# Kernel tuning notes

Measured on AMD Instinct MI355X. Metric: run time of the kernel, lower is better.

## Reference

```python
import jax, jax.numpy as jnp
import numpy as np

D_MODEL = 1024
NUM_HEADS = 16
HEAD_DIM = D_MODEL // NUM_HEADS
SCALE = HEAD_DIM ** -0.5


def setup_inputs() -> dict:
    key = jax.random.key(0)
    ks = jax.random.split(key, 5)
    B, N = 2, 2048
    x = jax.random.normal(ks[0], (B, N, D_MODEL), dtype=jnp.float32)
    # Linear params, torch layout: weight [out, in], bias [out]
    w_qkv = jax.random.normal(ks[1], (3 * D_MODEL, D_MODEL), dtype=jnp.float32) * (D_MODEL ** -0.5)
    b_qkv = jax.random.normal(ks[2], (3 * D_MODEL,), dtype=jnp.float32) * 0.02
    w_proj = jax.random.normal(ks[3], (D_MODEL, D_MODEL), dtype=jnp.float32) * (D_MODEL ** -0.5)
    b_proj = jax.random.normal(ks[4], (D_MODEL,), dtype=jnp.float32) * 0.02
    return {"x": x, "w_qkv": w_qkv, "b_qkv": b_qkv, "w_proj": w_proj, "b_proj": b_proj}


def reference(x, w_qkv, b_qkv, w_proj, b_proj):
    B, N, C = x.shape
    qkv = x @ w_qkv.T + b_qkv                      # [B, N, 3C]
    qkv = qkv.reshape(B, N, 3, NUM_HEADS, HEAD_DIM)
    qkv = jnp.transpose(qkv, (2, 0, 3, 1, 4))      # [3, B, H, N, d]
    q, k, v = qkv[0], qkv[1], qkv[2]
    attn = jnp.einsum('bhnd,bhmd->bhnm', q, k) * SCALE  # [B, H, N, N]
    attn = jax.nn.softmax(attn, axis=-1)
    # dropout is identity in eval mode
    out = jnp.einsum('bhnm,bhmd->bhnd', attn, v)   # [B, H, N, d]
    out = jnp.transpose(out, (0, 2, 1, 3)).reshape(B, N, C)
    return out @ w_proj.T + b_proj
```

## Files before the change

kernel.cpp:

```cpp
#include <hip/hip_runtime.h>

typedef short short8 __attribute__((ext_vector_type(8)));
typedef short short4v __attribute__((ext_vector_type(4)));
typedef float f32x4 __attribute__((ext_vector_type(4)));
typedef float float4v __attribute__((ext_vector_type(4)));
typedef int int4v __attribute__((ext_vector_type(4)));
typedef int int2v __attribute__((ext_vector_type(2)));

__device__ __forceinline__ short f2bf(float f) {
  union { float f; unsigned u; } v; v.f = f;
  unsigned r = v.u + 0x7FFFu + ((v.u >> 16) & 1u);
  return (short)(r >> 16);
}

__device__ __forceinline__ unsigned cvtpk_bf16(float lo, float hi) {
  unsigned r;
  asm("v_cvt_pk_bf16_f32 %0, %1, %2" : "=v"(r) : "v"(lo), "v"(hi));
  return r;
}

#define GLD16(gp, lp)                                                   \
  __builtin_amdgcn_global_load_lds(                                     \
      (const __attribute__((address_space(1))) void*)(gp),              \
      (__attribute__((address_space(3))) void*)(lp), 16, 0, 0)

#define QSCALE 0.18033688011112042f

__global__ __launch_bounds__(256) void cvt_all(
    const float* __restrict__ x, const float* __restrict__ wq, const float* __restrict__ wp,
    short* __restrict__ xb, short* __restrict__ wqb, short* __restrict__ wpb) {
  int i = blockIdx.x * 256 + threadIdx.x;
  const float* s; short* d; int off;
  if (i < 1048576)      { s = x;  d = xb;  off = i; }
  else if (i < 1835008) { s = wq; d = wqb; off = i - 1048576; }
  else                  { s = wp; d = wpb; off = i - 1835008; }
  float4v v = ((const float4v*)s)[off];
  short4v o;
  o.x = f2bf(v.x); o.y = f2bf(v.y); o.z = f2bf(v.z); o.w = f2bf(v.w);
  ((short4v*)d)[off] = o;
}

template <int MODE>
__global__ __launch_bounds__(256, 3) void gemm_bt(
    const short* __restrict__ A, const short* __restrict__ Bw,
    const float* __restrict__ bias,
    short* __restrict__ qo, short* __restrict__ ko, short* __restrict__ vto,
    float* __restrict__ outf) {
  __shared__ short As[3][128 * 32];
  __shared__ short Bs[3][128 * 32];
  const int t = threadIdx.x;
  const int lane = t & 63, wid = t >> 6;
  const int g = lane >> 4, l15 = lane & 15;
  const int wr = (wid >> 1) * 64, wc = (wid & 1) * 64;
  const int bid = blockIdx.x;
  const int bm0 = ((bid & 7) * 4 + ((bid >> 3) & 3)) * 128;
  const int bn0 = (bid >> 5) * 128;

  const int sr = t >> 2;
  const int csrc = (t & 3) ^ ((t >> 3) & 3);

  const int gx = (g ^ ((l15 >> 1) & 3)) << 4;
  int aoff[4], boff[4];
#pragma unroll
  for (int f = 0; f < 4; ++f) {
    aoff[f] = (wr + f * 16 + l15) * 64 + gx;
    boff[f] = (wc + f * 16 + l15) * 64 + gx;
  }

  f32x4 acc[4][4] = {};

  auto stage = [&](int offB, int k0) {
#pragma unroll
    for (int i = 0; i < 2; ++i) {
      int row = i * 64 + sr;
      char* ldsA = (char*)&As[0][0] + offB + (i * 256 + (t & ~63)) * 16;
      char* ldsB = (char*)&Bs[0][0] + offB + (i * 256 + (t & ~63)) * 16;
      GLD16(A + (size_t)(bm0 + row) * 1024 + k0 + csrc * 8, ldsA);
      GLD16(Bw + (size_t)(bn0 + row) * 1024 + k0 + csrc * 8, ldsB);
    }
  };

  stage(0, 0);
  stage(8192, 32);
  stage(16384, 64);
  int off = 0;

  for (int it = 0; it < 32; ++it) {
    if (it < 30)       asm volatile("s_waitcnt vmcnt(8)" ::: "memory");
    else if (it == 30) asm volatile("s_waitcnt vmcnt(4)" ::: "memory");
    else               asm volatile("s_waitcnt vmcnt(0)" ::: "memory");
    __builtin_amdgcn_s_barrier();
    __builtin_amdgcn_sched_barrier(0);
    const char* AsB = (const char*)&As[0][0] + off;
    const char* BsB = (const char*)&Bs[0][0] + off;
    short8 a[4], b[4];
#pragma unroll
    for (int mi = 0; mi < 4; ++mi) a[mi] = *(const short8*)(AsB + aoff[mi]);
#pragma unroll
    for (int ni = 0; ni < 4; ++ni) b[ni] = *(const short8*)(BsB + boff[ni]);
#pragma unroll
    for (int mi = 0; mi < 4; ++mi)
#pragma unroll
      for (int ni = 0; ni < 4; ++ni)
        acc[mi][ni] = __builtin_amdgcn_mfma_f32_16x16x32_bf16(a[mi], b[ni], acc[mi][ni], 0, 0, 0);
    __builtin_amdgcn_sched_barrier(0);
    __builtin_amdgcn_s_barrier();
    __builtin_amdgcn_sched_barrier(0);
    if (it + 3 < 32) stage(off, (it + 3) * 32);
    off = (off == 16384) ? 0 : off + 8192;
  }

  if constexpr (MODE == 0) {
    const int which = bn0 >> 10;
    if (which == 2) {
#pragma unroll
      for (int mi = 0; mi < 4; ++mi) {
#pragma unroll
        for (int ni = 0; ni < 4; ++ni) {
          int gcol = bn0 + wc + ni * 16 + l15;
          int w1 = gcol & 1023;
          int h = w1 >> 6, dd = w1 & 63;
          float bv = bias[gcol];
          int grow0 = bm0 + wr + mi * 16 + g * 4;
          int b_ = grow0 >> 11, n0 = grow0 & 2047;
          int bh = b_ * 16 + h;
          int nl = n0 & 63;
          int np = (n0 & ~63) | (nl & 32) | ((nl & 12) << 1) | ((nl & 16) >> 2);
          int2v pk;
          pk.x = (int)cvtpk_bf16(acc[mi][ni][0] + bv, acc[mi][ni][1] + bv);
          pk.y = (int)cvtpk_bf16(acc[mi][ni][2] + bv, acc[mi][ni][3] + bv);
          *(int2v*)(vto + ((size_t)bh * 64 + dd) * 2048 + np) = pk;
        }
      }
    } else {
      short* dst = (which == 0) ? qo : ko;
      const float sc = (which == 0) ? QSCALE : 1.0f;
#pragma unroll
      for (int mi = 0; mi < 4; ++mi) {
#pragma unroll
        for (int ni = 0; ni < 4; ++ni) {
          int gcol = bn0 + wc + ni * 16 + l15;
          int w1 = gcol & 1023;
          int h = w1 >> 6, dd = w1 & 63;
          float bv = bias[gcol];
#pragma unroll
          for (int r = 0; r < 4; ++r) {
            int grow = bm0 + wr + mi * 16 + g * 4 + r;
            int b_ = grow >> 11, n = grow & 2047;
            int bh = b_ * 16 + h;
            dst[((size_t)bh * 2048 + n) * 64 + dd] = f2bf((acc[mi][ni][r] + bv) * sc);
          }
        }
      }
    }
  } else {
#pragma unroll
    for (int mi = 0; mi < 4; ++mi) {
#pragma unroll
      for (int ni = 0; ni < 4; ++ni) {
        int gcol = bn0 + wc + ni * 16 + l15;
        float bv = bias[gcol];
#pragma unroll
        for (int r = 0; r < 4; ++r) {
          int grow = bm0 + wr + mi * 16 + g * 4 + r;
          outf[(size_t)grow * 1024 + gcol] = acc[mi][ni][r] + bv;
        }
      }
    }
  }
}

__global__ __launch_bounds__(256, 2) void attn_fused(
    const short* __restrict__ Qg, const short* __restrict__ Kg,
    const short* __restrict__ Vtg, short* __restrict__ AO) {
  __shared__ short Ks[4][64 * 64];
  __shared__ short Vs[4][64 * 64];
  const int bid = blockIdx.x;
  const int bh = bid & 31, qt = bid >> 5;
  const int t = threadIdx.x, wid = t >> 6, lane = t & 63;
  const int g = lane >> 4, l15 = lane & 15;
  const int q0w = qt * 128 + wid * 32;
  const short* qb = Qg + ((size_t)bh * 2048 + q0w) * 64;
  const short* kb = Kg + (size_t)bh * 2048 * 64;
  const short* vb = Vtg + (size_t)bh * 64 * 2048;

  const int srow = t >> 3;
  const int ssub = (t & 7) ^ (srow & 7);
  const short* ksrc0 = kb + srow * 64 + ssub * 8;
  const short* vsrc0 = vb + (size_t)srow * 2048 + ssub * 8;

  const int swz = (l15 & 7) << 4;
  int foff[2][4];
#pragma unroll
  for (int kk = 0; kk < 2; ++kk)
#pragma unroll
    for (int f = 0; f < 4; ++f)
      foff[kk][f] = ((f * 16 + l15) * 128 + kk * 64 + g * 16) ^ swz;

  short8 bq[2][2];
#pragma unroll
  for (int qf = 0; qf < 2; ++qf)
#pragma unroll
    for (int kk = 0; kk < 2; ++kk)
      bq[qf][kk] = *(const short8*)(qb + (qf * 16 + l15) * 64 + kk * 32 + g * 8);

  auto stageP = [&](int buf, int p) {
    const int n0 = p * 128;
#pragma unroll
    for (int sub = 0; sub < 2; ++sub) {
      const int nn = n0 + sub * 64;
      char* ldsK = (char*)&Ks[buf * 2 + sub][0] + wid * 1024;
      char* ldsV = (char*)&Vs[buf * 2 + sub][0] + wid * 1024;
#pragma unroll
      for (int i = 0; i < 2; ++i) {
        GLD16(ksrc0 + (size_t)(nn + i * 32) * 64, ldsK + i * 4096);
        GLD16(vsrc0 + (size_t)i * 32 * 2048 + nn, ldsV + i * 4096);
      }
    }
  };

  stageP(0, 0);
  stageP(1, 1);

  f32x4 acc[2][4] = {};
  float mrun[2] = {-3.0e38f, -3.0e38f}, lrun[2] = {0.f, 0.f};

  for (int p = 0; p < 16; ++p) {
    if (p == 15) asm volatile("s_waitcnt vmcnt(0)" ::: "memory");
    else         asm volatile("s_waitcnt vmcnt(8)" ::: "memory");
    __builtin_amdgcn_s_barrier();
    __builtin_amdgcn_sched_barrier(0);
    const int buf = p & 1;

#pragma unroll
    for (int sub = 0; sub < 2; ++sub) {
      const char* KsB = (const char*)&Ks[buf * 2 + sub][0];
      const char* VsB = (const char*)&Vs[buf * 2 + sub][0];

      f32x4 s[2][4] = {};
#pragma unroll
      for (int kk = 0; kk < 2; ++kk) {
        short8 ak[4];
#pragma unroll
        for (int kf = 0; kf < 4; ++kf) ak[kf] = *(const short8*)(KsB + foff[kk][kf]);
#pragma unroll
        for (int kf = 0; kf < 4; ++kf)
#pragma unroll
          for (int qf = 0; qf < 2; ++qf)
            s[qf][kf] = __builtin_amdgcn_mfma_f32_16x16x32_bf16(ak[kf], bq[qf][kk], s[qf][kf], 0, 0, 0);
      }

      float pm[2];
#pragma unroll
      for (int qf = 0; qf < 2; ++qf) {
        float m0 = fmaxf(s[qf][0][0], s[qf][0][1]);
        m0 = fmaxf(fmaxf(m0, s[qf][0][2]), s[qf][0][3]);
#pragma unroll
        for (int kf = 1; kf < 4; ++kf) {
          m0 = fmaxf(fmaxf(m0, s[qf][kf][0]), s[qf][kf][1]);
          m0 = fmaxf(fmaxf(m0, s[qf][kf][2]), s[qf][kf][3]);
        }
        float x = fmaxf(m0, __shfl_xor(m0, 16));
        pm[qf] = fmaxf(x, __shfl_xor(x, 32));
      }

      if (!__all((pm[0] - mrun[0] <= 8.f) && (pm[1] - mrun[1] <= 8.f))) {
#pragma unroll
        for (int qf = 0; qf < 2; ++qf) {
          float mn = fmaxf(mrun[qf], pm[qf]);
          float alpha = __builtin_amdgcn_exp2f(mrun[qf] - mn);
          mrun[qf] = mn;
          lrun[qf] *= alpha;
#pragma unroll
          for (int df = 0; df < 4; ++df)
#pragma unroll
            for (int r = 0; r < 4; ++r) acc[qf][df][r] *= alpha;
        }
      }

      unsigned wpk[2][4][2];
#pragma unroll
      for (int qf = 0; qf < 2; ++qf) {
        float rs = 0.f;
        float pp[4][4];
#pragma unroll
        for (int kf = 0; kf < 4; ++kf)
#pragma unroll
          for (int r = 0; r < 4; ++r) {
            pp[kf][r] = __builtin_amdgcn_exp2f(s[qf][kf][r] - mrun[qf]);
            rs += pp[kf][r];
          }
        rs += __shfl_xor(rs, 16);
        rs += __shfl_xor(rs, 32);
        lrun[qf] += rs;
#pragma unroll
        for (int kf = 0; kf < 4; ++kf)
#pragma unroll
          for (int h = 0; h < 2; ++h)
            wpk[qf][kf][h] = cvtpk_bf16(pp[kf][2 * h], pp[kf][2 * h + 1]);
      }

#pragma unroll
      for (int kk = 0; kk < 2; ++kk) {
        short8 av[4];
#pragma unroll
        for (int df = 0; df < 4; ++df) av[df] = *(const short8*)(VsB + foff[kk][df]);
#pragma unroll
        for (int qf = 0; qf < 2; ++qf) {
          union { int4v i; short8 s; } pv;
          pv.i[0] = (int)wpk[qf][2 * kk][0];
          pv.i[1] = (int)wpk[qf][2 * kk][1];
          pv.i[2] = (int)wpk[qf][2 * kk + 1][0];
          pv.i[3] = (int)wpk[qf][2 * kk + 1][1];
#pragma unroll
          for (int df = 0; df < 4; ++df)
            acc[qf][df] = __builtin_amdgcn_mfma_f32_16x16x32_bf16(av[df], pv.s, acc[qf][df], 0, 0, 0);
        }
      }
    }

    __builtin_amdgcn_sched_barrier(0);
    __builtin_amdgcn_s_barrier();
    __builtin_amdgcn_sched_barrier(0);
    if (p + 2 < 16) stageP(buf, p + 2);
  }

  const int b_ = bh >> 4, h = bh & 15;
#pragma unroll
  for (int qf = 0; qf < 2; ++qf) {
    const float inv = 1.0f / lrun[qf];
    short* outp = AO + ((size_t)b_ * 2048 + q0w + qf * 16 + l15) * 1024 + h * 64 + g * 4;
#pragma unroll
    for (int df = 0; df < 4; ++df) {
      short4v o;
#pragma unroll
      for (int r = 0; r < 4; ++r) o[r] = f2bf(acc[qf][df][r] * inv);
      *(short4v*)(outp + df * 16) = o;
    }
  }
}

extern "C" void kernel_launch(void* const* d_in, const int* in_sizes, int n_in,
                              void* d_out, int out_size, void* d_ws, size_t ws_size,
                              hipStream_t stream) {
  const float* x = (const float*)d_in[0];
  const float* w_qkv = (const float*)d_in[1];
  const float* b_qkv = (const float*)d_in[2];
  const float* w_proj = (const float*)d_in[3];
  const float* b_proj = (const float*)d_in[4];
  float* out = (float*)d_out;
  char* ws = (char*)d_ws;

  short* xb    = (short*)(ws + (size_t)0);
  short* wqkvb = (short*)(ws + ((size_t)8 << 20));
  short* wprojb= (short*)(ws + ((size_t)14 << 20));
  short* qb    = (short*)(ws + ((size_t)16 << 20));
  short* kb    = (short*)(ws + ((size_t)24 << 20));
  short* vtb   = (short*)(ws + ((size_t)32 << 20));
  short* aob   = (short*)(ws + ((size_t)40 << 20));

  cvt_all<<<8192, 256, 0, stream>>>(x, w_qkv, w_proj, xb, wqkvb, wprojb);
  gemm_bt<0><<<768, 256, 0, stream>>>(xb, wqkvb, b_qkv, qb, kb, vtb, nullptr);
  attn_fused<<<512, 256, 0, stream>>>(qb, kb, vtb, aob);
  gemm_bt<1><<<256, 256, 0, stream>>>(aob, wprojb, b_proj, nullptr, nullptr, nullptr, out);
}
```

Baseline: 115.7 us.

## Split attention KV sequence across wave pairs and merge partial softmax in LDS

Doubles the attention block to 512 threads, with each pair of waves sharing the same 32 queries but handling opposite halves of the key/value sequence (split-K flash attention). K loads are issued by waves 0-3 and V loads by waves 4-7. At the end, partial accumulators and running max/sum are exchanged through LDS and merged with rescaling. The aim is more waves in flight to hide latency and shorter per-wave serial loops. The cost is an extra LDS merge step, and the larger block with 64KB of shared memory may limit how many blocks fit per CU.

```diff
diff --git a/kernel.cpp b/kernel.cpp
--- a/kernel.cpp
+++ b/kernel.cpp
@@ -170,24 +170,26 @@
   }
 }
 
-__global__ __launch_bounds__(256, 2) void attn_fused(
+__global__ __launch_bounds__(512, 4) void attn_fused(
     const short* __restrict__ Qg, const short* __restrict__ Kg,
     const short* __restrict__ Vtg, short* __restrict__ AO) {
-  __shared__ short Ks[4][64 * 64];
-  __shared__ short Vs[4][64 * 64];
+  __shared__ char smem[65536];
+#define KSB(hf, buf) (smem + ((hf) * 2 + (buf)) * 8192)
+#define VSB(hf, buf) (smem + 32768 + ((hf) * 2 + (buf)) * 8192)
   const int bid = blockIdx.x;
   const int bh = bid & 31, qt = bid >> 5;
   const int t = threadIdx.x, wid = t >> 6, lane = t & 63;
   const int g = lane >> 4, l15 = lane & 15;
-  const int q0w = qt * 128 + wid * 32;
+  const int qg = wid >> 1, hf = wid & 1;
+  const int q0w = qt * 128 + qg * 32;
   const short* qb = Qg + ((size_t)bh * 2048 + q0w) * 64;
   const short* kb = Kg + (size_t)bh * 2048 * 64;
   const short* vb = Vtg + (size_t)bh * 64 * 2048;
 
-  const int srow = t >> 3;
-  const int ssub = (t & 7) ^ (srow & 7);
-  const short* ksrc0 = kb + srow * 64 + ssub * 8;
-  const short* vsrc0 = vb + (size_t)srow * 2048 + ssub * 8;
+  const int sr = (t & 255) >> 3;
+  const int ssub = (t & 7) ^ ((t >> 3) & 7);
+  const short* ksrc0 = kb + sr * 64 + ssub * 8;
+  const short* vsrc0 = vb + (size_t)sr * 2048 + ssub * 8;
 
   const int swz = (l15 & 7) << 4;
   int foff[2][4];
@@ -205,17 +207,20 @@
       bq[qf][kk] = *(const short8*)(qb + (qf * 16 + l15) * 64 + kk * 32 + g * 8);
 
   auto stageP = [&](int buf, int p) {
-    const int n0 = p * 128;
-#pragma unroll
-    for (int sub = 0; sub < 2; ++sub) {
-      const int nn = n0 + sub * 64;
-      char* ldsK = (char*)&Ks[buf * 2 + sub][0] + wid * 1024;
-      char* ldsV = (char*)&Vs[buf * 2 + sub][0] + wid * 1024;
-#pragma unroll
-      for (int i = 0; i < 2; ++i) {
-        GLD16(ksrc0 + (size_t)(nn + i * 32) * 64, ldsK + i * 4096);
-        GLD16(vsrc0 + (size_t)i * 32 * 2048 + nn, ldsV + i * 4096);
-      }
+    if (wid < 4) {
+#pragma unroll
+      for (int h2 = 0; h2 < 2; ++h2)
+#pragma unroll
+        for (int i = 0; i < 2; ++i)
+          GLD16(ksrc0 + (size_t)(h2 * 1024 + p * 64 + i * 32) * 64,
+                KSB(h2, buf) + i * 4096 + wid * 1024);
+    } else {
+#pragma unroll
+      for (int h2 = 0; h2 < 2; ++h2)
+#pragma unroll
+        for (int i = 0; i < 2; ++i)
+          GLD16(vsrc0 + (size_t)(i * 32) * 2048 + h2 * 1024 + p * 64,
+                VSB(h2, buf) + i * 4096 + (wid - 4) * 1024);
     }
   };
 
@@ -227,117 +232,138 @@
 
   for (int p = 0; p < 16; ++p) {
     if (p == 15) asm volatile("s_waitcnt vmcnt(0)" ::: "memory");
-    else         asm volatile("s_waitcnt vmcnt(8)" ::: "memory");
+    else         asm volatile("s_waitcnt vmcnt(4)" ::: "memory");
     __builtin_amdgcn_s_barrier();
     __builtin_amdgcn_sched_barrier(0);
-    const int buf = p & 1;
-
-#pragma unroll
-    for (int sub = 0; sub < 2; ++sub) {
-      const char* KsB = (const char*)&Ks[buf * 2 + sub][0];
-      const char* VsB = (const char*)&Vs[buf * 2 + sub][0];
-
-      f32x4 s[2][4] = {};
-#pragma unroll
-      for (int kk = 0; kk < 2; ++kk) {
-        short8 ak[4];
-#pragma unroll
-        for (int kf = 0; kf < 4; ++kf) ak[kf] = *(const short8*)(KsB + foff[kk][kf]);
-#pragma unroll
-        for (int kf = 0; kf < 4; ++kf)
-#pragma unroll
-          for (int qf = 0; qf < 2; ++qf)
-            s[qf][kf] = __builtin_amdgcn_mfma_f32_16x16x32_bf16(ak[kf], bq[qf][kk], s[qf][kf], 0, 0, 0);
-      }
-
-      float pm[2];
+    const char* KsB = (const char*)KSB(hf, p & 1);
+    const char* VsB = (const char*)VSB(hf, p & 1);
+
+    f32x4 s[2][4] = {};
+#pragma unroll
+    for (int kk = 0; kk < 2; ++kk) {
+      short8 ak[4];
+#pragma unroll
+      for (int kf = 0; kf < 4; ++kf) ak[kf] = *(const short8*)(KsB + foff[kk][kf]);
+#pragma unroll
+      for (int kf = 0; kf < 4; ++kf)
+#pragma unroll
+        for (int qf = 0; qf < 2; ++qf)
+          s[qf][kf] = __builtin_amdgcn_mfma_f32_16x16x32_bf16(ak[kf], bq[qf][kk], s[qf][kf], 0, 0, 0);
+    }
+
+    float pm[2];
+#pragma unroll
+    for (int qf = 0; qf < 2; ++qf) {
+      float m0 = fmaxf(s[qf][0][0], s[qf][0][1]);
+      m0 = fmaxf(fmaxf(m0, s[qf][0][2]), s[qf][0][3]);
+#pragma unroll
+      for (int kf = 1; kf < 4; ++kf) {
+        m0 = fmaxf(fmaxf(m0, s[qf][kf][0]), s[qf][kf][1]);
+        m0 = fmaxf(fmaxf(m0, s[qf][kf][2]), s[qf][kf][3]);
+      }
+      float x = fmaxf(m0, __shfl_xor(m0, 16));
+      pm[qf] = fmaxf(x, __shfl_xor(x, 32));
+    }
+
+    if (!__all((pm[0] - mrun[0] <= 8.f) && (pm[1] - mrun[1] <= 8.f))) {
 #pragma unroll
       for (int qf = 0; qf < 2; ++qf) {
-        float m0 = fmaxf(s[qf][0][0], s[qf][0][1]);
-        m0 = fmaxf(fmaxf(m0, s[qf][0][2]), s[qf][0][3]);
-#pragma unroll
-        for (int kf = 1; kf < 4; ++kf) {
-          m0 = fmaxf(fmaxf(m0, s[qf][kf][0]), s[qf][kf][1]);
-          m0 = fmaxf(fmaxf(m0, s[qf][kf][2]), s[qf][kf][3]);
+        float mn = fmaxf(mrun[qf], pm[qf]);
+        float alpha = __builtin_amdgcn_exp2f(mrun[qf] - mn);
+        mrun[qf] = mn;
+        lrun[qf] *= alpha;
+#pragma unroll
+        for (int df = 0; df < 4; ++df)
+#pragma unroll
+          for (int r = 0; r < 4; ++r) acc[qf][df][r] *= alpha;
+      }
+    }
+
+    unsigned wpk[2][4][2];
+#pragma unroll
+    for (int qf = 0; qf < 2; ++qf) {
+      float rs = 0.f;
+      float pp[4][4];
+#pragma unroll
+      for (int kf = 0; kf < 4; ++kf)
+#pragma unroll
+        for (int r = 0; r < 4; ++r) {
+          pp[kf][r] = __builtin_amdgcn_exp2f(s[qf][kf][r] - mrun[qf]);
+          rs += pp[kf][r];
         }
-        float x = fmaxf(m0, __shfl_xor(m0, 16));
-        pm[qf] = fmaxf(x, __shfl_xor(x, 32));
-      }
-
-      if (!__all((pm[0] - mrun[0] <= 8.f) && (pm[1] - mrun[1] <= 8.f))) {
-#pragma unroll
-        for (int qf = 0; qf < 2; ++qf) {
-          float mn = fmaxf(mrun[qf], pm[qf]);
-          float alpha = __builtin_amdgcn_exp2f(mrun[qf] - mn);
-          mrun[qf] = mn;
-          lrun[qf] *= alpha;
-#pragma unroll
-          for (int df = 0; df < 4; ++df)
-#pragma unroll
-            for (int r = 0; r < 4; ++r) acc[qf][df][r] *= alpha;
-        }
-      }
-
-      unsigned wpk[2][4][2];
+      rs += __shfl_xor(rs, 16);
+      rs += __shfl_xor(rs, 32);
+      lrun[qf] += rs;
+#pragma unroll
+      for (int kf = 0; kf < 4; ++kf)
+#pragma unroll
+        for (int h2 = 0; h2 < 2; ++h2)
+          wpk[qf][kf][h2] = cvtpk_bf16(pp[kf][2 * h2], pp[kf][2 * h2 + 1]);
+    }
+
+#pragma unroll
+    for (int kk = 0; kk < 2; ++kk) {
+      short8 av[4];
+#pragma unroll
+      for (int df = 0; df < 4; ++df) av[df] = *(const short8*)(VsB + foff[kk][df]);
 #pragma unroll
       for (int qf = 0; qf < 2; ++qf) {
-        float rs = 0.f;
-        float pp[4][4];
-#pragma unroll
-        for (int kf = 0; kf < 4; ++kf)
-#pragma unroll
-          for (int r = 0; r < 4; ++r) {
-            pp[kf][r] = __builtin_amdgcn_exp2f(s[qf][kf][r] - mrun[qf]);
-            rs += pp[kf][r];
-          }
-        rs += __shfl_xor(rs, 16);
-        rs += __shfl_xor(rs, 32);
-        lrun[qf] += rs;
-#pragma unroll
-        for (int kf = 0; kf < 4; ++kf)
-#pragma unroll
-          for (int h = 0; h < 2; ++h)
-            wpk[qf][kf][h] = cvtpk_bf16(pp[kf][2 * h], pp[kf][2 * h + 1]);
-      }
-
-#pragma unroll
-      for (int kk = 0; kk < 2; ++kk) {
-        short8 av[4];
-#pragma unroll
-        for (int df = 0; df < 4; ++df) av[df] = *(const short8*)(VsB + foff[kk][df]);
-#pragma unroll
-        for (int qf = 0; qf < 2; ++qf) {
-          union { int4v i; short8 s; } pv;
-          pv.i[0] = (int)wpk[qf][2 * kk][0];
-          pv.i[1] = (int)wpk[qf][2 * kk][1];
-          pv.i[2] = (int)wpk[qf][2 * kk + 1][0];
-          pv.i[3] = (int)wpk[qf][2 * kk + 1][1];
-#pragma unroll
-          for (int df = 0; df < 4; ++df)
-            acc[qf][df] = __builtin_amdgcn_mfma_f32_16x16x32_bf16(av[df], pv.s, acc[qf][df], 0, 0, 0);
-        }
+        union { int4v i; short8 s; } pv;
+        pv.i[0] = (int)wpk[qf][2 * kk][0];
+        pv.i[1] = (int)wpk[qf][2 * kk][1];
+        pv.i[2] = (int)wpk[qf][2 * kk + 1][0];
+        pv.i[3] = (int)wpk[qf][2 * kk + 1][1];
+#pragma unroll
+        for (int df = 0; df < 4; ++df)
+          acc[qf][df] = __builtin_amdgcn_mfma_f32_16x16x32_bf16(av[df], pv.s, acc[qf][df], 0, 0, 0);
       }
     }
 
     __builtin_amdgcn_sched_barrier(0);
     __builtin_amdgcn_s_barrier();
     __builtin_amdgcn_sched_barrier(0);
-    if (p + 2 < 16) stageP(buf, p + 2);
-  }
-
-  const int b_ = bh >> 4, h = bh & 15;
-#pragma unroll
-  for (int qf = 0; qf < 2; ++qf) {
-    const float inv = 1.0f / lrun[qf];
-    short* outp = AO + ((size_t)b_ * 2048 + q0w + qf * 16 + l15) * 1024 + h * 64 + g * 4;
-#pragma unroll
-    for (int df = 0; df < 4; ++df) {
-      short4v o;
-#pragma unroll
-      for (int r = 0; r < 4; ++r) o[r] = f2bf(acc[qf][df][r] * inv);
-      *(short4v*)(outp + df * 16) = o;
-    }
-  }
+    if (p + 2 < 16) stageP(p & 1, p + 2);
+  }
+
+  float* cacc = (float*)smem;
+  float* cml = (float*)(smem + 4 * 64 * 33 * 4);
+  __syncthreads();
+  if (hf == 1) {
+    float* pa = cacc + (qg * 64 + lane) * 33;
+#pragma unroll
+    for (int qf = 0; qf < 2; ++qf)
+#pragma unroll
+      for (int df = 0; df < 4; ++df)
+#pragma unroll
+        for (int r = 0; r < 4; ++r) pa[qf * 16 + df * 4 + r] = acc[qf][df][r];
+    float* pl = cml + (qg * 64 + lane) * 4;
+    pl[0] = mrun[0]; pl[1] = lrun[0]; pl[2] = mrun[1]; pl[3] = lrun[1];
+  }
+  __syncthreads();
+  if (hf == 0) {
+    const float* pa = cacc + (qg * 64 + lane) * 33;
+    const float* pl = cml + (qg * 64 + lane) * 4;
+    const int b_ = bh >> 4, h = bh & 15;
+#pragma unroll
+    for (int qf = 0; qf < 2; ++qf) {
+      float m1 = pl[qf * 2], l1 = pl[qf * 2 + 1];
+      float M = fmaxf(mrun[qf], m1);
+      float a0 = __builtin_amdgcn_exp2f(mrun[qf] - M);
+      float a1 = __builtin_amdgcn_exp2f(m1 - M);
+      float inv = 1.0f / (lrun[qf] * a0 + l1 * a1);
+      short* outp = AO + ((size_t)b_ * 2048 + q0w + qf * 16 + l15) * 1024 + h * 64 + g * 4;
+#pragma unroll
+      for (int df = 0; df < 4; ++df) {
+        short4v o;
+#pragma unroll
+        for (int r = 0; r < 4; ++r)
+          o[r] = f2bf((acc[qf][df][r] * a0 + pa[qf * 16 + df * 4 + r] * a1) * inv);
+        *(short4v*)(outp + df * 16) = o;
+      }
+    }
+  }
+#undef KSB
+#undef VSB
 }
 
 extern "C" void kernel_launch(void* const* d_in, const int* in_sizes, int n_in,
@@ -361,6 +387,6 @@
 
   cvt_all<<<8192, 256, 0, stream>>>(x, w_qkv, w_proj, xb, wqkvb, wprojb);
   gemm_bt<0><<<768, 256, 0, stream>>>(xb, wqkvb, b_qkv, qb, kb, vtb, nullptr);
-  attn_fused<<<512, 256, 0, stream>>>(qb, kb, vtb, aob);
+  attn_fused<<<512, 512, 0, stream>>>(qb, kb, vtb, aob);
   gemm_bt<1><<<256, 256, 0, stream>>>(aob, wprojb, b_proj, nullptr, nullptr, nullptr, out);
 }
```

New measurement: 135.6 us. 17.3% more time.

## Use 256x256-tile 512-thread GEMM for QKV projection with double-buffered LDS

Applied to the files above, without the earlier changes.

Replaces the 128x128-tile QKV GEMM with a new kernel using 256x256 tiles, 8 waves, K-step 64 and a 128KB double-buffered LDS pipeline. Staging of the next k-tile is interleaved with the MFMA sub-loops, with explicit vmcnt waits and setprio around the MFMAs. The larger tile raises arithmetic intensity and cuts global traffic per FLOP. The grid drops to 192 blocks, below the 256 CUs, so the GPU is under-occupied and fewer blocks hide latency. The output projection is split out into its own non-templated kernel.

```diff
diff --git a/kernel.cpp b/kernel.cpp
--- a/kernel.cpp
+++ b/kernel.cpp
@@ -40,12 +40,134 @@
   ((short4v*)d)[off] = o;
 }
 
-template <int MODE>
-__global__ __launch_bounds__(256, 3) void gemm_bt(
+__global__ __launch_bounds__(512, 2) void gemm256(
     const short* __restrict__ A, const short* __restrict__ Bw,
     const float* __restrict__ bias,
-    short* __restrict__ qo, short* __restrict__ ko, short* __restrict__ vto,
-    float* __restrict__ outf) {
+    short* __restrict__ qo, short* __restrict__ ko, short* __restrict__ vto) {
+  __shared__ char lds[131072];
+  const int t = threadIdx.x;
+  const int lane = t & 63, wid = t >> 6;
+  const int g = lane >> 4, l15 = lane & 15;
+  const int wr = wid >> 2, wc = wid & 3;
+  const int bid = blockIdx.x;
+  const int bm0 = ((bid & 7) * 2 + ((bid >> 3) & 1)) * 256;
+  const int bn0 = (bid >> 4) * 256;
+
+  const int srow = t >> 3;
+  const int ssub = (t & 7) ^ ((t >> 3) & 7);
+
+  const int swz = (l15 & 7) << 4;
+  int inrow[2];
+  inrow[0] = (g * 16) ^ swz;
+  inrow[1] = (64 + g * 16) ^ swz;
+  const int bRow0 = (wc & 1) * 64;
+
+  f32x4 acc[8][4] = {};
+
+  auto stageHT = [&](int b, int kt, int ht) {
+    const int isB = ht >> 1, hh = ht & 1;
+    const short* mat = isB ? Bw : A;
+    const int base = isB ? bn0 : bm0;
+    const short* src = mat + (size_t)(base + hh * 128 + srow) * 1024 + kt * 64 + ssub * 8;
+    char* dst = lds + b * 65536 + isB * 32768 + hh * 16384 + t * 16;
+    GLD16(src, dst);
+    GLD16(src + 64 * 1024, dst + 8192);
+  };
+
+#pragma unroll
+  for (int ht = 0; ht < 4; ++ht) stageHT(0, 0, ht);
+
+  for (int k = 0; k < 16; ++k) {
+    const int buf = k & 1;
+    const char* Ab = lds + buf * 65536 + wr * 16384;
+    const char* Bb = lds + buf * 65536 + 32768 + (wc >> 1) * 16384;
+    short8 bB[4][2];
+#pragma unroll
+    for (int mp = 0; mp < 4; ++mp) {
+      if (k + 1 < 16) stageHT(buf ^ 1, k + 1, mp);
+      __builtin_amdgcn_sched_barrier(0);
+      if (mp == 0) {
+        if (k + 1 < 16) asm volatile("s_waitcnt vmcnt(2)" ::: "memory");
+        else            asm volatile("s_waitcnt vmcnt(0)" ::: "memory");
+        __builtin_amdgcn_s_barrier();
+        __builtin_amdgcn_sched_barrier(0);
+#pragma unroll
+        for (int n = 0; n < 4; ++n)
+#pragma unroll
+          for (int kk = 0; kk < 2; ++kk)
+            bB[n][kk] = *(const short8*)(Bb + (bRow0 + n * 16 + l15) * 128 + inrow[kk]);
+      }
+      short8 aA[2][2];
+#pragma unroll
+      for (int mm = 0; mm < 2; ++mm)
+#pragma unroll
+        for (int kk = 0; kk < 2; ++kk)
+          aA[mm][kk] = *(const short8*)(Ab + ((mp * 2 + mm) * 16 + l15) * 128 + inrow[kk]);
+      __builtin_amdgcn_s_setprio(1);
+#pragma unroll
+      for (int mm = 0; mm < 2; ++mm)
+#pragma unroll
+        for (int n = 0; n < 4; ++n)
+#pragma unroll
+          for (int kk = 0; kk < 2; ++kk)
+            acc[mp * 2 + mm][n] = __builtin_amdgcn_mfma_f32_16x16x32_bf16(
+                aA[mm][kk], bB[n][kk], acc[mp * 2 + mm][n], 0, 0, 0);
+      __builtin_amdgcn_s_setprio(0);
+      if (mp == 3) {
+        __builtin_amdgcn_sched_barrier(0);
+        __builtin_amdgcn_s_barrier();
+        __builtin_amdgcn_sched_barrier(0);
+      }
+    }
+  }
+
+  const int which = bn0 >> 10;
+  if (which == 2) {
+#pragma unroll
+    for (int m = 0; m < 8; ++m) {
+#pragma unroll
+      for (int n = 0; n < 4; ++n) {
+        int gcol = bn0 + wc * 64 + n * 16 + l15;
+        int w1 = gcol & 1023;
+        int h = w1 >> 6, dd = w1 & 63;
+        float bv = bias[gcol];
+        int grow0 = bm0 + wr * 128 + m * 16 + g * 4;
+        int b_ = grow0 >> 11, n0 = grow0 & 2047;
+        int bh = b_ * 16 + h;
+        int nl = n0 & 63;
+        int np = (n0 & ~63) | (nl & 32) | ((nl & 12) << 1) | ((nl & 16) >> 2);
+        int2v pk;
+        pk.x = (int)cvtpk_bf16(acc[m][n][0] + bv, acc[m][n][1] + bv);
+        pk.y = (int)cvtpk_bf16(acc[m][n][2] + bv, acc[m][n][3] + bv);
+        *(int2v*)(vto + ((size_t)bh * 64 + dd) * 2048 + np) = pk;
+      }
+    }
+  } else {
+    short* dst = (which == 0) ? qo : ko;
+    const float sc = (which == 0) ? QSCALE : 1.0f;
+#pragma unroll
+    for (int m = 0; m < 8; ++m) {
+#pragma unroll
+      for (int n = 0; n < 4; ++n) {
+        int gcol = bn0 + wc * 64 + n * 16 + l15;
+        int w1 = gcol & 1023;
+        int h = w1 >> 6, dd = w1 & 63;
+        float bv = bias[gcol];
+#pragma unroll
+        for (int r = 0; r < 4; ++r) {
+          int grow = bm0 + wr * 128 + m * 16 + g * 4 + r;
+          int b_ = grow >> 11, n2 = grow & 2047;
+          int bh = b_ * 16 + h;
+          dst[((size_t)bh * 2048 + n2) * 64 + dd] = f2bf((acc[m][n][r] + bv) * sc);
+        }
+      }
+    }
+  }
+}
+
+__global__ __launch_bounds__(256, 3) void gemm_proj(
+    const short* __restrict__ A, const short* __restrict__ Bw,
+    const float* __restrict__ bias, float* __restrict__ outf) {
   __shared__ short As[3][128 * 32];
   __shared__ short Bs[3][128 * 32];
   const int t = threadIdx.x;
@@ -110,61 +232,16 @@
     off = (off == 16384) ? 0 : off + 8192;
   }
 
-  if constexpr (MODE == 0) {
-    const int which = bn0 >> 10;
-    if (which == 2) {
-#pragma unroll
-      for (int mi = 0; mi < 4; ++mi) {
-#pragma unroll
-        for (int ni = 0; ni < 4; ++ni) {
-          int gcol = bn0 + wc + ni * 16 + l15;
-          int w1 = gcol & 1023;
-          int h = w1 >> 6, dd = w1 & 63;
-          float bv = bias[gcol];
-          int grow0 = bm0 + wr + mi * 16 + g * 4;
-          int b_ = grow0 >> 11, n0 = grow0 & 2047;
-          int bh = b_ * 16 + h;
-          int nl = n0 & 63;
-          int np = (n0 & ~63) | (nl & 32) | ((nl & 12) << 1) | ((nl & 16) >> 2);
-          int2v pk;
-          pk.x = (int)cvtpk_bf16(acc[mi][ni][0] + bv, acc[mi][ni][1] + bv);
-          pk.y = (int)cvtpk_bf16(acc[mi][ni][2] + bv, acc[mi][ni][3] + bv);
-          *(int2v*)(vto + ((size_t)bh * 64 + dd) * 2048 + np) = pk;
-        }
-      }
-    } else {
-      short* dst = (which == 0) ? qo : ko;
-      const float sc = (which == 0) ? QSCALE : 1.0f;
-#pragma unroll
-      for (int mi = 0; mi < 4; ++mi) {
-#pragma unroll
-        for (int ni = 0; ni < 4; ++ni) {
-          int gcol = bn0 + wc + ni * 16 + l15;
-          int w1 = gcol & 1023;
-          int h = w1 >> 6, dd = w1 & 63;
-          float bv = bias[gcol];
-#pragma unroll
-          for (int r = 0; r < 4; ++r) {
-            int grow = bm0 + wr + mi * 16 + g * 4 + r;
-            int b_ = grow >> 11, n = grow & 2047;
-            int bh = b_ * 16 + h;
-            dst[((size_t)bh * 2048 + n) * 64 + dd] = f2bf((acc[mi][ni][r] + bv) * sc);
-          }
-        }
-      }
-    }
-  } else {
-#pragma unroll
-    for (int mi = 0; mi < 4; ++mi) {
-#pragma unroll
-      for (int ni = 0; ni < 4; ++ni) {
-        int gcol = bn0 + wc + ni * 16 + l15;
-        float bv = bias[gcol];
-#pragma unroll
-        for (int r = 0; r < 4; ++r) {
-          int grow = bm0 + wr + mi * 16 + g * 4 + r;
-          outf[(size_t)grow * 1024 + gcol] = acc[mi][ni][r] + bv;
-        }
+#pragma unroll
+  for (int mi = 0; mi < 4; ++mi) {
+#pragma unroll
+    for (int ni = 0; ni < 4; ++ni) {
+      int gcol = bn0 + wc + ni * 16 + l15;
+      float bv = bias[gcol];
+#pragma unroll
+      for (int r = 0; r < 4; ++r) {
+        int grow = bm0 + wr + mi * 16 + g * 4 + r;
+        outf[(size_t)grow * 1024 + gcol] = acc[mi][ni][r] + bv;
       }
     }
   }
@@ -360,7 +437,7 @@
   short* aob   = (short*)(ws + ((size_t)40 << 20));
 
   cvt_all<<<8192, 256, 0, stream>>>(x, w_qkv, w_proj, xb, wqkvb, wprojb);
-  gemm_bt<0><<<768, 256, 0, stream>>>(xb, wqkvb, b_qkv, qb, kb, vtb, nullptr);
+  gemm256<<<192, 512, 0, stream>>>(xb, wqkvb, b_qkv, qb, kb, vtb);
   attn_fused<<<512, 256, 0, stream>>>(qb, kb, vtb, aob);
-  gemm_bt<1><<<256, 256, 0, stream>>>(aob, wprojb, b_proj, nullptr, nullptr, nullptr, out);
-}
+  gemm_proj<<<256, 256, 0, stream>>>(aob, wprojb, b_proj, out);
+}
```

New measurement: 115.3 us, median of 2. Within noise of the previous version (-0.3%).
